# Kernel tuning notes

Measured on AMD Instinct MI355X. Metric: run time of the kernel, lower is better.

The kernel has to match this reference:

```python
import jax, jax.numpy as jnp
import numpy as np

B, S, D_IN, D_OUT, H = 1, 4096, 1024, 1024, 16
HD = D_OUT // H


def setup_inputs() -> dict:
    key = jax.random.key(0)
    ks = jax.random.split(key, 6)
    sc = 0.02
    return {
        "x": jax.random.normal(ks[0], (B, S, D_IN), dtype=jnp.float32),
        "Wq": jax.random.normal(ks[1], (D_IN, D_OUT), dtype=jnp.float32) * sc,
        "Wk": jax.random.normal(ks[2], (D_IN, D_OUT), dtype=jnp.float32) * sc,
        "Wv": jax.random.normal(ks[3], (D_IN, D_OUT), dtype=jnp.float32) * sc,
        "Wo": jax.random.normal(ks[4], (D_OUT, D_OUT), dtype=jnp.float32) * sc,
        "bo": jnp.zeros((D_OUT,), dtype=jnp.float32),
    }


def reference(x, Wq, Wk, Wv, Wo, bo):
    b, n, _ = x.shape
    # QKV projections (no bias), split into heads: [b, h, n, hd]
    def heads(w):
        return (x @ w).reshape(b, n, H, HD).transpose(0, 2, 1, 3)
    q, k, v = heads(Wq), heads(Wk), heads(Wv)
    # scores [b, h, n, n], causal mask, scaled softmax (dropout p=0 -> identity)
    scores = jnp.einsum("bhqd,bhkd->bhqk", q, k)
    causal = jnp.tril(jnp.ones((n, n), dtype=bool))
    scores = jnp.where(causal, scores, -jnp.inf)
    attn = jax.nn.softmax(scores / jnp.sqrt(jnp.float32(HD)), axis=-1)
    ctx = jnp.einsum("bhqk,bhkd->bhqd", attn, v)
    ctx = ctx.transpose(0, 2, 1, 3).reshape(b, n, D_OUT)
    return ctx @ Wo + bo
```

## Files before the change

kernel.cpp:

```cpp
#include <hip/hip_runtime.h>
#include <hip/hip_bf16.h>
#include <stdint.h>


typedef __bf16 bf16;
typedef __bf16 bf16x4 __attribute__((ext_vector_type(4)));
typedef __bf16 bf16x8 __attribute__((ext_vector_type(8)));
typedef float  f32x4  __attribute__((ext_vector_type(4)));

#define MFMA32(a, b, c) __builtin_amdgcn_mfma_f32_16x16x32_bf16((a), (b), (c), 0, 0, 0)

static constexpr int S_LEN  = 4096;
static constexpr int DMODEL = 1024;
static constexpr int HDIM   = 64;
static constexpr int LDQK   = 2048;

#define GLOAD_LDS16(g, l)                                                      \
  __builtin_amdgcn_global_load_lds((__attribute__((address_space(1))) void*)(g), \
                                   (__attribute__((address_space(3))) void*)(l), 16, 0, 0)

__global__ __launch_bounds__(256) void preprocess(const float* __restrict__ x,
                                                  const float* __restrict__ Wq,
                                                  const float* __restrict__ Wk,
                                                  const float* __restrict__ Wv,
                                                  const float* __restrict__ Wo,
                                                  bf16* __restrict__ xb,
                                                  bf16* __restrict__ Wt,
                                                  bf16* __restrict__ Wot) {
  __shared__ float tile[64][65];
  const int t = threadIdx.x, b = blockIdx.x;
  if (b < 1024) {
#pragma unroll
    for (int i = 0; i < 4; i++) {
      int idx = b * 1024 + i * 256 + t;
      float4 v = ((const float4*)x)[idx];
      bf16x4 o;
      o[0] = (bf16)v.x; o[1] = (bf16)v.y; o[2] = (bf16)v.z; o[3] = (bf16)v.w;
      ((bf16x4*)xb)[idx] = o;
    }
    return;
  }
  const int id = b - 1024;
  const int wsel = id >> 8;
  const int t2 = id & 255;
  const int kb = (t2 & 15) * 64, nb = (t2 >> 4) * 64;
  const float* src = (wsel == 0) ? Wq : (wsel == 1) ? Wk : (wsel == 2) ? Wv : Wo;
  bf16* dst = (wsel < 3) ? (Wt + (size_t)wsel * 1024 * 1024) : Wot;
#pragma unroll
  for (int i = 0; i < 16; i++) {
    int idx = t + i * 256;
    int r = idx >> 6, c = idx & 63;
    tile[r][c] = src[(size_t)(kb + r) * 1024 + nb + c];
  }
  __syncthreads();
#pragma unroll
  for (int i = 0; i < 16; i++) {
    int idx = t + i * 256;
    int cc = idx >> 6, rr = idx & 63;
    dst[(size_t)(nb + cc) * 1024 + kb + rr] = (bf16)tile[rr][cc];
  }
}

__global__ __launch_bounds__(256) void gemm_qkv(const bf16* __restrict__ A,
                                                const bf16* __restrict__ Bt,
                                                bf16* __restrict__ QK,
                                                bf16* __restrict__ Vt) {
  __shared__ bf16 lsA[128 * 32];
  __shared__ bf16 lsB[128 * 32];
  const int tid = threadIdx.x, w = tid >> 6, lane = tid & 63;
  const int l15 = lane & 15, quad = lane >> 4;
  const int m0 = blockIdx.x * 128, n0 = blockIdx.y * 128;
  const int wm = (w >> 1) * 64, wn = (w & 1) * 64;
  const int rowA = lane >> 2;
  const int colk = (((lane & 3) ^ ((lane >> 3) & 3))) * 8;
  const int rsl = (l15 >> 1) & 3;

  f32x4 acc[4][4] = {};

  for (int k0 = 0; k0 < 1024; k0 += 32) {
    __syncthreads();
#pragma unroll
    for (int i = 0; i < 2; i++) {
      int s = w * 2 + i;
      const bf16* ga = A + (size_t)(m0 + s * 16 + rowA) * 1024 + k0 + colk;
      GLOAD_LDS16(ga, lsA + s * 512);
      const bf16* gb = Bt + (size_t)(n0 + s * 16 + rowA) * 1024 + k0 + colk;
      GLOAD_LDS16(gb, lsB + s * 512);
    }
    __syncthreads();

    bf16x8 af[4], bfr[4];
#pragma unroll
    for (int r = 0; r < 4; r++)
      af[r] = *(const bf16x8*)(lsA + (wm + r * 16 + l15) * 32 + (quad ^ rsl) * 8);
#pragma unroll
    for (int c = 0; c < 4; c++)
      bfr[c] = *(const bf16x8*)(lsB + (wn + c * 16 + l15) * 32 + (quad ^ rsl) * 8);
#pragma unroll
    for (int r = 0; r < 4; r++)
#pragma unroll
      for (int c = 0; c < 4; c++)
        acc[r][c] = MFMA32(af[r], bfr[c], acc[r][c]);
  }

  if (n0 < 2048) {
#pragma unroll
    for (int r = 0; r < 4; r++) {
#pragma unroll
      for (int c = 0; c < 4; c++) {
        int col = n0 + wn + c * 16 + l15;
        float scale = (col < 1024) ? 0.18033688f : 1.0f;
#pragma unroll
        for (int e = 0; e < 4; e++) {
          int row = m0 + wm + r * 16 + quad * 4 + e;
          QK[(size_t)row * LDQK + col] = (bf16)(acc[r][c][e] * scale);
        }
      }
    }
  } else {
#pragma unroll
    for (int r = 0; r < 4; r++) {
#pragma unroll
      for (int c = 0; c < 4; c++) {
        int vcol = (n0 - 2048) + wn + c * 16 + l15;
        int row0 = m0 + wm + r * 16 + quad * 4;
        bf16x4 pk;
#pragma unroll
        for (int e = 0; e < 4; e++) pk[e] = (bf16)acc[r][c][e];
        *(bf16x4*)(Vt + (size_t)vcol * S_LEN + row0) = pk;
      }
    }
  }
}

__global__ __launch_bounds__(256, 2) void flash_attn(const bf16* __restrict__ QK,
                                                     const bf16* __restrict__ Vt,
                                                     bf16* __restrict__ Ctx) {
  __shared__ float Obuf[4][16][68];
  __shared__ float Lbuf[4][4][64];
  const int tid = threadIdx.x, w = tid >> 6, lane = tid & 63;
  const int l15 = lane & 15, quad = lane >> 4;
  const int i = blockIdx.x;
  const int head = (i & 7) + 8 * ((i >> 3) & 1);
  const int qt_raw = i >> 4;
  const int qb = (qt_raw < 32) ? qt_raw : (95 - qt_raw);
  const int hq = head * HDIM;
  const int krow0 = w * 32 + ((l15 >> 2) << 3) + (l15 & 3);

  const int T = (qb >> 1) + 1;

  bf16x8 qf[4][2];
#pragma unroll
  for (int qg = 0; qg < 4; qg++)
#pragma unroll
    for (int kk = 0; kk < 2; kk++)
      qf[qg][kk] = *(const bf16x8*)(QK + (size_t)(qb * 64 + qg * 16 + l15) * LDQK +
                                    hq + kk * 32 + quad * 8);

  f32x4 oacc[4][4] = {};
  float lsum[4] = {0.f, 0.f, 0.f, 0.f};

  auto load_k = [&](int j, bf16x8 (&kf)[2][2]) {
#pragma unroll
    for (int c = 0; c < 2; c++)
#pragma unroll
      for (int kk = 0; kk < 2; kk++)
        kf[c][kk] = *(const bf16x8*)(QK + (size_t)(j * 128 + krow0 + 4 * c) * LDQK +
                                     DMODEL + hq + kk * 32 + quad * 8);
  };
  auto load_v = [&](int j, bf16x8 (&vf)[4]) {
#pragma unroll
    for (int dg = 0; dg < 4; dg++)
      vf[dg] = *(const bf16x8*)(Vt + (size_t)(hq + dg * 16 + l15) * S_LEN +
                                j * 128 + w * 32 + quad * 8);
  };
  auto compute = [&](int j, bf16x8 (&kf)[2][2], bf16x8 (&vf)[4]) {
    f32x4 sacc[2][4] = {};
    __builtin_amdgcn_s_setprio(1);
#pragma unroll
    for (int kk = 0; kk < 2; kk++)
#pragma unroll
      for (int c = 0; c < 2; c++)
#pragma unroll
        for (int qg = 0; qg < 4; qg++)
          sacc[c][qg] = MFMA32(kf[c][kk], qf[qg][kk], sacc[c][qg]);
    __builtin_amdgcn_s_setprio(0);

    bf16x8 pfr[4];
    if (j == T - 1) {
      const int kb0 = j * 128 + w * 32 + quad * 8;
#pragma unroll
      for (int qg = 0; qg < 4; qg++) {
        const int qrow = qb * 64 + qg * 16 + l15;
        bf16x8 pb;
#pragma unroll
        for (int c = 0; c < 2; c++)
#pragma unroll
          for (int e = 0; e < 4; e++) {
            float s = sacc[c][qg][e];
            if (kb0 + 4 * c + e > qrow) s = -1e30f;
            float pv = __builtin_amdgcn_exp2f(s);
            lsum[qg] += pv;
            pb[c * 4 + e] = (bf16)pv;
          }
        pfr[qg] = pb;
      }
    } else {
#pragma unroll
      for (int qg = 0; qg < 4; qg++) {
        bf16x8 pb;
#pragma unroll
        for (int c = 0; c < 2; c++)
#pragma unroll
          for (int e = 0; e < 4; e++) {
            float pv = __builtin_amdgcn_exp2f(sacc[c][qg][e]);
            lsum[qg] += pv;
            pb[c * 4 + e] = (bf16)pv;
          }
        pfr[qg] = pb;
      }
    }

    __builtin_amdgcn_s_setprio(1);
#pragma unroll
    for (int qg = 0; qg < 4; qg++)
#pragma unroll
      for (int dg = 0; dg < 4; dg++)
        oacc[qg][dg] = MFMA32(pfr[qg], vf[dg], oacc[qg][dg]);
    __builtin_amdgcn_s_setprio(0);
  };

  bf16x8 kfA[2][2], vfA[4], kfB[2][2], vfB[4];
  load_k(0, kfA); load_v(0, vfA);
  for (int j = 0; j < T; j += 2) {
    if (j + 1 < T) { load_k(j + 1, kfB); load_v(j + 1, vfB); }
    compute(j, kfA, vfA);
    if (j + 2 < T) { load_k(j + 2, kfA); load_v(j + 2, vfA); }
    if (j + 1 < T) compute(j + 1, kfB, vfB);
  }

#pragma unroll
  for (int qg = 0; qg < 4; qg++)
    Lbuf[w][quad][qg * 16 + l15] = lsum[qg];

  const int row = tid >> 4;
  const int col = (tid & 15) * 4;
  for (int qg = 0; qg < 4; qg++) {
#pragma unroll
    for (int dg = 0; dg < 4; dg++)
#pragma unroll
      for (int e = 0; e < 4; e++)
        Obuf[w][quad * 4 + e][dg * 16 + l15] = oacc[qg][dg][e];
    __syncthreads();
    f32x4 os = {};
#pragma unroll
    for (int ww = 0; ww < 4; ww++)
      os += *(const f32x4*)&Obuf[ww][row][col];
    float lr = 0.f;
#pragma unroll
    for (int ww = 0; ww < 4; ww++)
#pragma unroll
      for (int qq = 0; qq < 4; qq++)
        lr += Lbuf[ww][qq][qg * 16 + row];
    const float linv = 1.f / lr;
    bf16x4 ob;
#pragma unroll
    for (int e2 = 0; e2 < 4; e2++) ob[e2] = (bf16)(os[e2] * linv);
    *(bf16x4*)(Ctx + (size_t)(qb * 64 + qg * 16 + row) * DMODEL + hq + col) = ob;
    __syncthreads();
  }
}

__global__ __launch_bounds__(256) void gemm_out(const bf16* __restrict__ A,
                                                const bf16* __restrict__ Bt,
                                                float* __restrict__ C,
                                                const float* __restrict__ bias) {
  __shared__ bf16 lsA[64 * 32];
  __shared__ bf16 lsB[128 * 32];
  const int tid = threadIdx.x, w = tid >> 6, lane = tid & 63;
  const int l15 = lane & 15, quad = lane >> 4;
  const int m0 = blockIdx.x * 64, n0 = blockIdx.y * 128;
  const int wm = (w >> 1) * 32, wn = (w & 1) * 64;
  const int rowA = lane >> 2;
  const int colk = (((lane & 3) ^ ((lane >> 3) & 3))) * 8;
  const int rsl = (l15 >> 1) & 3;

  f32x4 acc[2][4] = {};

  for (int k0 = 0; k0 < 1024; k0 += 32) {
    __syncthreads();
#pragma unroll
    for (int i = 0; i < 3; i++) {
      int s = w * 3 + i;
      if (s < 4) {
        const bf16* ga = A + (size_t)(m0 + s * 16 + rowA) * 1024 + k0 + colk;
        GLOAD_LDS16(ga, lsA + s * 512);
      } else {
        const bf16* gb = Bt + (size_t)(n0 + (s - 4) * 16 + rowA) * 1024 + k0 + colk;
        GLOAD_LDS16(gb, lsB + (s - 4) * 512);
      }
    }
    __syncthreads();

    bf16x8 af[2], bfr[4];
#pragma unroll
    for (int r = 0; r < 2; r++)
      af[r] = *(const bf16x8*)(lsA + (wm + r * 16 + l15) * 32 + (quad ^ rsl) * 8);
#pragma unroll
    for (int c = 0; c < 4; c++)
      bfr[c] = *(const bf16x8*)(lsB + (wn + c * 16 + l15) * 32 + (quad ^ rsl) * 8);
#pragma unroll
    for (int r = 0; r < 2; r++)
#pragma unroll
      for (int c = 0; c < 4; c++)
        acc[r][c] = MFMA32(af[r], bfr[c], acc[r][c]);
  }

#pragma unroll
  for (int r = 0; r < 2; r++) {
#pragma unroll
    for (int c = 0; c < 4; c++) {
      int col = n0 + wn + c * 16 + l15;
#pragma unroll
      for (int e = 0; e < 4; e++) {
        int row = m0 + wm + r * 16 + quad * 4 + e;
        C[(size_t)row * 1024 + col] = acc[r][c][e] + bias[col];
      }
    }
  }
}

extern "C" void kernel_launch(void* const* d_in, const int* in_sizes, int n_in,
                              void* d_out, int out_size, void* d_ws, size_t ws_size,
                              hipStream_t stream) {
  const float* x  = (const float*)d_in[0];
  const float* Wq = (const float*)d_in[1];
  const float* Wk = (const float*)d_in[2];
  const float* Wv = (const float*)d_in[3];
  const float* Wo = (const float*)d_in[4];
  const float* bo = (const float*)d_in[5];

  char* ws = (char*)d_ws;
  bf16* xb  = (bf16*)(ws);
  bf16* Wt  = (bf16*)(ws + (8u  << 20));
  bf16* Wot = (bf16*)(ws + (14u << 20));
  bf16* QK  = (bf16*)(ws + (16u << 20));
  bf16* Vt  = (bf16*)(ws + (32u << 20));
  bf16* Ctx = (bf16*)(ws + (40u << 20));

  preprocess<<<2048, 256, 0, stream>>>(x, Wq, Wk, Wv, Wo, xb, Wt, Wot);
  gemm_qkv<<<dim3(32, 24), 256, 0, stream>>>(xb, Wt, QK, Vt);
  flash_attn<<<1024, 256, 0, stream>>>(QK, Vt, Ctx);
  gemm_out<<<dim3(64, 8), 256, 0, stream>>>(Ctx, Wot, (float*)d_out, bo);
}
```

Baseline: 206.6 us.

## Store K and V in fragment-ordered layout so attention loads are fully coalesced

The QKV GEMM epilogue now writes K and V into a per-head, per-wave fragment layout that matches how flash attention lanes consume them, and Q goes to its own buffer. Each lane in the attention kernel can then read its bf16x8 operand from a contiguous lane*8 offset instead of doing strided row gathers. The cost moves to the GEMM epilogue, where K stores become scattered 2-byte writes. The flash_attn kernel's global memory access pattern, which dominates runtime, is what this change targets.

```diff
diff --git a/kernel.cpp b/kernel.cpp
--- a/kernel.cpp
+++ b/kernel.cpp
@@ -13,7 +13,6 @@
 static constexpr int S_LEN  = 4096;
 static constexpr int DMODEL = 1024;
 static constexpr int HDIM   = 64;
-static constexpr int LDQK   = 2048;
 
 #define GLOAD_LDS16(g, l)                                                      \
   __builtin_amdgcn_global_load_lds((__attribute__((address_space(1))) void*)(g), \
@@ -63,8 +62,9 @@
 
 __global__ __launch_bounds__(256) void gemm_qkv(const bf16* __restrict__ A,
                                                 const bf16* __restrict__ Bt,
-                                                bf16* __restrict__ QK,
-                                                bf16* __restrict__ Vt) {
+                                                bf16* __restrict__ Qb,
+                                                bf16* __restrict__ Kf,
+                                                bf16* __restrict__ Vf) {
   __shared__ bf16 lsA[128 * 32];
   __shared__ bf16 lsB[128 * 32];
   const int tid = threadIdx.x, w = tid >> 6, lane = tid & 63;
@@ -103,38 +103,56 @@
         acc[r][c] = MFMA32(af[r], bfr[c], acc[r][c]);
   }
 
-  if (n0 < 2048) {
+  if (n0 < 1024) {
 #pragma unroll
     for (int r = 0; r < 4; r++) {
 #pragma unroll
       for (int c = 0; c < 4; c++) {
         int col = n0 + wn + c * 16 + l15;
-        float scale = (col < 1024) ? 0.18033688f : 1.0f;
 #pragma unroll
         for (int e = 0; e < 4; e++) {
           int row = m0 + wm + r * 16 + quad * 4 + e;
-          QK[(size_t)row * LDQK + col] = (bf16)(acc[r][c][e] * scale);
+          Qb[(size_t)row * 1024 + col] = (bf16)(acc[r][c][e] * 0.18033688f);
         }
       }
     }
+  } else if (n0 < 2048) {
+    const int h  = (n0 - 1024 + wn) >> 6;
+    const int g0 = (m0 + wm) >> 5;
+    bf16* base = Kf + (size_t)(h * 128 + g0) * 2048 +
+                 (quad & 1) * 1024 + (l15 >> 3) * 128 + (quad >> 1) * 32 + (l15 & 7);
+#pragma unroll
+    for (int r = 0; r < 4; r++) {
+#pragma unroll
+      for (int c = 0; c < 4; c++) {
+#pragma unroll
+        for (int e = 0; e < 4; e++) {
+          base[(r >> 1) * 2048 + (r & 1) * 64 + (c >> 1) * 512 + (c & 1) * 256 + e * 8] =
+              (bf16)acc[r][c][e];
+        }
+      }
+    }
   } else {
+    const int h  = (n0 - 2048 + wn) >> 6;
+    const int g0 = (m0 + wm) >> 5;
+    bf16* base = Vf + (size_t)(h * 128 + g0) * 2048 +
+                 (quad >> 1) * 128 + l15 * 8 + (quad & 1) * 4;
 #pragma unroll
     for (int r = 0; r < 4; r++) {
 #pragma unroll
       for (int c = 0; c < 4; c++) {
-        int vcol = (n0 - 2048) + wn + c * 16 + l15;
-        int row0 = m0 + wm + r * 16 + quad * 4;
         bf16x4 pk;
 #pragma unroll
         for (int e = 0; e < 4; e++) pk[e] = (bf16)acc[r][c][e];
-        *(bf16x4*)(Vt + (size_t)vcol * S_LEN + row0) = pk;
-      }
-    }
-  }
-}
-
-__global__ __launch_bounds__(256, 2) void flash_attn(const bf16* __restrict__ QK,
-                                                     const bf16* __restrict__ Vt,
+        *(bf16x4*)(base + (r >> 1) * 2048 + (r & 1) * 256 + c * 512) = pk;
+      }
+    }
+  }
+}
+
+__global__ __launch_bounds__(256, 2) void flash_attn(const bf16* __restrict__ Qb,
+                                                     const bf16* __restrict__ Kf,
+                                                     const bf16* __restrict__ Vf,
                                                      bf16* __restrict__ Ctx) {
   __shared__ float Obuf[4][16][68];
   __shared__ float Lbuf[4][4][64];
@@ -145,16 +163,18 @@
   const int qt_raw = i >> 4;
   const int qb = (qt_raw < 32) ? qt_raw : (95 - qt_raw);
   const int hq = head * HDIM;
-  const int krow0 = w * 32 + ((l15 >> 2) << 3) + (l15 & 3);
 
   const int T = (qb >> 1) + 1;
 
+  const bf16* Kw = Kf + (size_t)(head * 128 + w) * 2048 + lane * 8;
+  const bf16* Vw = Vf + (size_t)(head * 128 + w) * 2048 + lane * 8;
+
   bf16x8 qf[4][2];
 #pragma unroll
   for (int qg = 0; qg < 4; qg++)
 #pragma unroll
     for (int kk = 0; kk < 2; kk++)
-      qf[qg][kk] = *(const bf16x8*)(QK + (size_t)(qb * 64 + qg * 16 + l15) * LDQK +
+      qf[qg][kk] = *(const bf16x8*)(Qb + (size_t)(qb * 64 + qg * 16 + l15) * 1024 +
                                     hq + kk * 32 + quad * 8);
 
   f32x4 oacc[4][4] = {};
@@ -165,14 +185,12 @@
     for (int c = 0; c < 2; c++)
 #pragma unroll
       for (int kk = 0; kk < 2; kk++)
-        kf[c][kk] = *(const bf16x8*)(QK + (size_t)(j * 128 + krow0 + 4 * c) * LDQK +
-                                     DMODEL + hq + kk * 32 + quad * 8);
+        kf[c][kk] = *(const bf16x8*)(Kw + j * 8192 + c * 1024 + kk * 512);
   };
   auto load_v = [&](int j, bf16x8 (&vf)[4]) {
 #pragma unroll
     for (int dg = 0; dg < 4; dg++)
-      vf[dg] = *(const bf16x8*)(Vt + (size_t)(hq + dg * 16 + l15) * S_LEN +
-                                j * 128 + w * 32 + quad * 8);
+      vf[dg] = *(const bf16x8*)(Vw + j * 8192 + dg * 512);
   };
   auto compute = [&](int j, bf16x8 (&kf)[2][2], bf16x8 (&vf)[4]) {
     f32x4 sacc[2][4] = {};
@@ -344,12 +362,13 @@
   bf16* xb  = (bf16*)(ws);
   bf16* Wt  = (bf16*)(ws + (8u  << 20));
   bf16* Wot = (bf16*)(ws + (14u << 20));
-  bf16* QK  = (bf16*)(ws + (16u << 20));
-  bf16* Vt  = (bf16*)(ws + (32u << 20));
+  bf16* Qb  = (bf16*)(ws + (16u << 20));
+  bf16* Kf  = (bf16*)(ws + (24u << 20));
+  bf16* Vf  = (bf16*)(ws + (32u << 20));
   bf16* Ctx = (bf16*)(ws + (40u << 20));
 
   preprocess<<<2048, 256, 0, stream>>>(x, Wq, Wk, Wv, Wo, xb, Wt, Wot);
-  gemm_qkv<<<dim3(32, 24), 256, 0, stream>>>(xb, Wt, QK, Vt);
-  flash_attn<<<1024, 256, 0, stream>>>(QK, Vt, Ctx);
+  gemm_qkv<<<dim3(32, 24), 256, 0, stream>>>(xb, Wt, Qb, Kf, Vf);
+  flash_attn<<<1024, 256, 0, stream>>>(Qb, Kf, Vf, Ctx);
   gemm_out<<<dim3(64, 8), 256, 0, stream>>>(Ctx, Wot, (float*)d_out, bo);
 }
```

New measurement: 178.2 us. 13.7% less time.
